# Kernel optimization log

Hardware: AMD Instinct MI355X
Metric: run time of the kernel (lower is better)

Reference implementation:

```python
import jax, jax.numpy as jnp
import numpy as np

NEG_INF_SCALE = -1e9


def multihead(q_in, kv_in, W, b, mask):
    # W: [3, H, d, dh] (q, k, v); b: [3, H, dh]
    q = jnp.einsum('bsd,hdk->bhsk', q_in, W[0]) + b[0][None, :, None, :]
    k = jnp.einsum('bsd,hdk->bhsk', kv_in, W[1]) + b[1][None, :, None, :]
    v = jnp.einsum('bsd,hdk->bhsk', kv_in, W[2]) + b[2][None, :, None, :]
    dh = q.shape[-1]
    scores = jnp.einsum('bhqd,bhkd->bhqk', q, k) / jnp.sqrt(jnp.float32(dh))
    if mask is not None:
        scores = scores + mask * NEG_INF_SCALE  # mask==1 at disallowed positions
    attn = jax.nn.softmax(scores, axis=-1)
    out = jnp.einsum('bhqk,bhkd->bhqd', attn, v)
    B, H, S, DH = out.shape
    # concat of per-head outputs along last axis == transpose + reshape
    return out.transpose(0, 2, 1, 3).reshape(B, S, H * DH)


def setup_inputs() -> dict:
    key = jax.random.key(0)
    ks = jax.random.split(key, 8)
    B, S, D, H, DH, DFF = 8, 1024, 1024, 16, 64, 2048
    sc_in = 1.0 / np.sqrt(D)
    sc_ff = 1.0 / np.sqrt(DFF)
    de_x = jax.random.normal(ks[0], (B, S, D), jnp.float32)
    en_x = jax.random.normal(ks[1], (B, S, D), jnp.float32)
    # causal mask: 1 at masked (future) positions
    mask = jnp.triu(jnp.ones((S, S), jnp.float32), k=1)
    attn1_w = jax.random.normal(ks[2], (3, H, D, DH), jnp.float32) * sc_in
    attn1_b = jnp.zeros((3, H, DH), jnp.float32)
    attn2_w = jax.random.normal(ks[3], (3, H, D, DH), jnp.float32) * sc_in
    attn2_b = jnp.zeros((3, H, DH), jnp.float32)
    ffn_w1 = jax.random.normal(ks[4], (D, DFF), jnp.float32) * sc_in
    ffn_b1 = jnp.zeros((DFF,), jnp.float32)
    ffn_w2 = jax.random.normal(ks[5], (DFF, D), jnp.float32) * sc_ff
    ffn_b2 = jnp.zeros((D,), jnp.float32)
    return {'de_x': de_x, 'en_x': en_x, 'mask': mask,
            'attn1_w': attn1_w, 'attn1_b': attn1_b,
            'attn2_w': attn2_w, 'attn2_b': attn2_b,
            'ffn_w1': ffn_w1, 'ffn_b1': ffn_b1,
            'ffn_w2': ffn_w2, 'ffn_b2': ffn_b2}


def reference(de_x, en_x, mask, attn1_w, attn1_b, attn2_w, attn2_b,
              ffn_w1, ffn_b1, ffn_w2, ffn_b2):
    # block 1: K=V=en_x, Q=de_x, masked (as in source: head(en_x, en_x, de_x, mask))
    h1 = multihead(de_x, en_x, attn1_w, attn1_b, mask)
    # block 2: K=V=en_x, Q=h1, no mask
    h2 = multihead(h1, en_x, attn2_w, attn2_b, None)
    # FCLayer(2048, d): d -> 2048 relu -> d
    y = jax.nn.relu(h2 @ ffn_w1 + ffn_b1) @ ffn_w2 + ffn_b2
    return y
```

## Files before the change

kernel.cpp:

```cpp
#include <hip/hip_runtime.h>

typedef unsigned short u16;
typedef __attribute__((ext_vector_type(8))) __bf16 bf16x8;
typedef __attribute__((ext_vector_type(4))) float f32x4;

__device__ __forceinline__ u16 f2bf(float f) {
    unsigned int u = __builtin_bit_cast(unsigned int, f);
    u = (u + 0x7fffu + ((u >> 16) & 1u)) >> 16;
    return (u16)u;
}

typedef __attribute__((address_space(1))) const void gv_t;
typedef __attribute__((address_space(3))) void lv_t;
__device__ __forceinline__ void gl_lds16(const void* g, void* l) {
    __builtin_amdgcn_global_load_lds((gv_t*)g, (lv_t*)l, 16, 0, 0);
}

__global__ __launch_bounds__(256) void cvt_bf16_k(const float* __restrict__ in,
                                                  u16* __restrict__ out, int n4) {
    int i = blockIdx.x * 256 + threadIdx.x;
    if (i >= n4) return;
    float4 f = ((const float4*)in)[i];
    ushort4 o;
    o.x = f2bf(f.x); o.y = f2bf(f.y); o.z = f2bf(f.z); o.w = f2bf(f.w);
    ((ushort4*)out)[i] = o;
}

__global__ __launch_bounds__(256) void pack_attn_w_k(const float* __restrict__ W,
                                                     u16* __restrict__ out) {
    int idx = blockIdx.x * 256 + threadIdx.x;
    int kk = idx & 63;
    int d  = (idx >> 6) & 1023;
    int h  = (idx >> 16) & 15;
    int p  = idx >> 20;
    out[p * 1048576 + (h * 64 + kk) * 1024 + d] = f2bf(W[idx]);
}

__global__ __launch_bounds__(256) void transpose_bf16_k(const float* __restrict__ in,
                                                        u16* __restrict__ out, int R, int C) {
    int idx = blockIdx.x * 256 + threadIdx.x;
    if (idx >= R * C) return;
    int r = idx / C, c = idx - r * C;
    out[c * R + r] = f2bf(in[idx]);
}

__device__ __forceinline__ void g256_core(const u16* __restrict__ Ab,
                                          const u16* __restrict__ Bb,
                                          int K, u16* __restrict__ As,
                                          u16* __restrict__ Bs,
                                          f32x4 (&acc)[8][4]) {
    const int tid = threadIdx.x, lane = tid & 63, wid = tid >> 6;
    const int wm = wid >> 2, wn = wid & 3;
    const int l15 = lane & 15, l4 = lane >> 4;
    const int gsw = (lane & 7) ^ ((lane >> 3) & 7);
    const int lr = lane >> 3;

    bf16x8 a[4][2], b[2][2];

#define STG(MATb, MATs, buf, half, kt) { \
    _Pragma("unroll") \
    for (int j = 0; j < 2; ++j) { \
        const int r = (half) * 128 + j * 64 + wid * 8; \
        gl_lds16(MATb + (size_t)(r + lr) * K + (kt) * 64 + gsw * 8, \
                 &MATs[(buf) * 16384 + r * 64]); \
    } }
#define LDA(buf, MLO) { \
    _Pragma("unroll") \
    for (int mf = 0; mf < 4; ++mf) \
    _Pragma("unroll") \
    for (int ks = 0; ks < 2; ++ks) \
        a[mf][ks] = *(const bf16x8*)&As[(buf) * 16384 \
            + (wm * 128 + ((MLO) + mf) * 16 + l15) * 64 \
            + (((ks * 4 + l4) ^ (l15 & 7)) * 8)]; \
    }
#define LDB(buf, NLO) { \
    _Pragma("unroll") \
    for (int nf = 0; nf < 2; ++nf) \
    _Pragma("unroll") \
    for (int ks = 0; ks < 2; ++ks) \
        b[nf][ks] = *(const bf16x8*)&Bs[(buf) * 16384 \
            + (wn * 64 + ((NLO) + nf) * 16 + l15) * 64 \
            + (((ks * 4 + l4) ^ (l15 & 7)) * 8)]; \
    }
#define MMA(MLO, NLO) { \
    __builtin_amdgcn_s_setprio(1); \
    _Pragma("unroll") \
    for (int mf = 0; mf < 4; ++mf) \
    _Pragma("unroll") \
    for (int nf = 0; nf < 2; ++nf) \
    _Pragma("unroll") \
    for (int ks = 0; ks < 2; ++ks) \
        acc[(MLO) + mf][(NLO) + nf] = __builtin_amdgcn_mfma_f32_16x16x32_bf16( \
            a[mf][ks], b[nf][ks], acc[(MLO) + mf][(NLO) + nf], 0, 0, 0); \
    __builtin_amdgcn_s_setprio(0); \
    }
#define BARR __builtin_amdgcn_s_barrier()
#define LGKM0 { asm volatile("s_waitcnt lgkmcnt(0)" ::: "memory"); \
                __builtin_amdgcn_sched_barrier(0); }
#define WTV2 asm volatile("s_waitcnt vmcnt(2)" ::: "memory")
#define WTV0 asm volatile("s_waitcnt vmcnt(0)" ::: "memory")

    const int NI = K >> 7;
    STG(Ab, As, 0, 0, 0); STG(Ab, As, 0, 1, 0);
    STG(Bb, Bs, 0, 0, 0); STG(Bb, Bs, 0, 1, 0);
    STG(Ab, As, 1, 0, 1);
    WTV2;
    BARR;

    for (int it = 0; it < NI; ++it) {
        const int t1 = 2 * it + 1, t2 = 2 * it + 2, t3 = 2 * it + 3;
        const bool nl = (it + 1 < NI);
        LDA(0, 0); LDB(0, 0);
        STG(Ab, As, 1, 1, t1);
        BARR; LGKM0; MMA(0, 0); BARR;
        LDB(0, 2);
        STG(Bb, Bs, 1, 0, t1);
        BARR; LGKM0; MMA(0, 2); BARR;
        LDA(0, 4); LDB(0, 0);
        STG(Bb, Bs, 1, 1, t1);
        BARR; LGKM0; MMA(4, 0); BARR;
        LDB(0, 2);
        if (nl) STG(Ab, As, 0, 0, t2);
        BARR; LGKM0; MMA(4, 2);
        if (nl) { WTV2; } else { WTV0; }
        BARR;
        LDA(1, 0); LDB(1, 0);
        if (nl) STG(Ab, As, 0, 1, t2);
        BARR; LGKM0; MMA(0, 0); BARR;
        LDB(1, 2);
        if (nl) STG(Bb, Bs, 0, 0, t2);
        BARR; LGKM0; MMA(0, 2); BARR;
        LDA(1, 4); LDB(1, 0);
        if (nl) STG(Bb, Bs, 0, 1, t2);
        BARR; LGKM0; MMA(4, 0); BARR;
        LDB(1, 2);
        if (nl) STG(Ab, As, 1, 0, t3);
        BARR; LGKM0; MMA(4, 2);
        if (nl) WTV2;
        BARR;
    }
#undef STG
#undef LDA
#undef LDB
#undef MMA
#undef BARR
#undef LGKM0
#undef WTV2
#undef WTV0
}

template <int MODE>
__global__ __launch_bounds__(512, 2) void gemm256_k(const u16* __restrict__ A,
        const u16* __restrict__ Bt, const float* __restrict__ bias,
        u16* __restrict__ Obf, float* __restrict__ Of,
        int M, int N, int K, float scale) {
    __shared__ u16 As[32768];
    __shared__ u16 Bs[32768];
    const int m0 = blockIdx.y * 256, n0 = blockIdx.x * 256;
    f32x4 acc[8][4] = {};
    g256_core(A + (size_t)m0 * K, Bt + (size_t)n0 * K, K, As, Bs, acc);

    const int lane = threadIdx.x & 63, wid = threadIdx.x >> 6;
    const int wm = wid >> 2, wn = wid & 3, l15 = lane & 15, l4 = lane >> 4;
    #pragma unroll
    for (int mf = 0; mf < 8; ++mf)
        #pragma unroll
        for (int nf = 0; nf < 4; ++nf) {
            int col = n0 + wn * 64 + nf * 16 + l15;
            float bv = bias[col];
            int row0 = m0 + wm * 128 + mf * 16 + l4 * 4;
            #pragma unroll
            for (int i = 0; i < 4; ++i) {
                float v = acc[mf][nf][i] + bv;
                if (MODE == 1) v = fmaxf(v, 0.f);
                v *= scale;
                if (MODE == 2) Of[(size_t)(row0 + i) * N + col] = v;
                else           Obf[(size_t)(row0 + i) * N + col] = f2bf(v);
            }
        }
}

__global__ __launch_bounds__(512, 2) void gemm256_proj_k(const u16* __restrict__ Ade,
        const u16* __restrict__ Aen, const u16* __restrict__ W,
        const float* __restrict__ b1, const float* __restrict__ b2,
        u16* __restrict__ Qb, u16* __restrict__ Kb1, u16* __restrict__ Vt1,
        u16* __restrict__ Kb2, u16* __restrict__ Vt2) {
    const int K = 1024;
    __shared__ u16 As[32768];
    __shared__ u16 Bs[32768];
    const int xt = blockIdx.x;
    const int n0 = (xt < 12 ? xt : xt + 4) * 256;
    const int seg = n0 >> 10;
    const int m0 = blockIdx.y * 256;
    const u16* A = (seg == 0) ? Ade : Aen;
    f32x4 acc[8][4] = {};
    g256_core(A + (size_t)m0 * K, W + (size_t)n0 * K, K, As, Bs, acc);

    const int lane = threadIdx.x & 63, wid = threadIdx.x >> 6;
    const int wm = wid >> 2, wn = wid & 3, l15 = lane & 15, l4 = lane >> 4;
    const float* bias = (seg < 3) ? (b1 + seg * 1024) : (b2 + (seg - 3) * 1024);
    const int isV = (seg == 2 || seg == 5);
    u16* Orow = (seg == 0) ? Qb : (seg == 1 ? Kb1 : Kb2);
    u16* Ovt  = (seg == 2) ? Vt1 : Vt2;
    const float scale = (seg == 0) ? 0.125f : 1.0f;

    #pragma unroll
    for (int mf = 0; mf < 8; ++mf)
        #pragma unroll
        for (int nf = 0; nf < 4; ++nf) {
            int colg = n0 + wn * 64 + nf * 16 + l15;
            int col = colg & 1023;
            float bv = bias[col];
            int row0 = m0 + wm * 128 + mf * 16 + l4 * 4;
            if (isV) {
                ushort4 o;
                o.x = f2bf(acc[mf][nf][0] + bv);
                o.y = f2bf(acc[mf][nf][1] + bv);
                o.z = f2bf(acc[mf][nf][2] + bv);
                o.w = f2bf(acc[mf][nf][3] + bv);
                size_t off = ((size_t)((row0 >> 10) * 16 + (col >> 6)) * 64
                              + (col & 63)) * 1024 + (row0 & 1023);
                *(ushort4*)&Ovt[off] = o;
            } else {
                #pragma unroll
                for (int i = 0; i < 4; ++i)
                    Orow[(size_t)(row0 + i) * 1024 + col] =
                        f2bf((acc[mf][nf][i] + bv) * scale);
            }
        }
}

template <int CAUSAL>
__global__ __launch_bounds__(256) void attn_k(const u16* __restrict__ Q,
                                              const u16* __restrict__ Kg_,
                                              const u16* __restrict__ Vt_,
                                              u16* __restrict__ O, int S) {
    const int HD = 1024;
    __shared__ u16 Kl[2][4096];
    __shared__ u16 Vl[2][4096];
    __shared__ u16 Pl[4][16 * 72];
    const int tid = threadIdx.x, lane = tid & 63, w = tid >> 6;
    const int qt = blockIdx.x, h = blockIdx.y, b = blockIdx.z;
    const u16* Qg  = Q   + ((size_t)b * S) * HD + h * 64;
    const u16* Kgp = Kg_ + ((size_t)b * S) * HD + h * 64;
    const u16* Vtp = Vt_ + (size_t)(b * 16 + h) * 64 * 1024;
    const int q0 = qt * 64 + w * 16;
    const int l15 = lane & 15, l4 = lane >> 4;
    const int sr = lane >> 3, sc = lane & 7;

    bf16x8 aq[2];
    #pragma unroll
    for (int kc = 0; kc < 2; ++kc)
        aq[kc] = *(const bf16x8*)&Qg[(size_t)(q0 + l15) * HD + kc * 32 + l4 * 8];

    f32x4 acc_o[4] = {};
    float mrow[4], lrow[4];
    #pragma unroll
    for (int i = 0; i < 4; ++i) { mrow[i] = -3.0e38f; lrow[i] = 0.f; }
    u16* Pw = Pl[w];

    const int nkb = CAUSAL ? (qt + 1) : (S / 64);

    {
        #pragma unroll
        for (int qq = 0; qq < 2; ++qq) {
            int rbase = w * 16 + qq * 8;
            int r = rbase + sr;
            int cs = sc ^ (r & 7);
            gl_lds16(Kgp + (size_t)r * HD + cs * 8, (void*)&Kl[0][rbase * 64]);
            gl_lds16(Vtp + (size_t)r * 1024 + cs * 8, (void*)&Vl[0][rbase * 64]);
        }
    }
    __syncthreads();

    int buf = 0;
    for (int kb = 0; kb < nkb; ++kb) {
        if (kb + 1 < nkb) {
            const int k0n = (kb + 1) * 64;
            #pragma unroll
            for (int qq = 0; qq < 2; ++qq) {
                int rbase = w * 16 + qq * 8;
                int r = rbase + sr;
                int cs = sc ^ (r & 7);
                gl_lds16(Kgp + (size_t)(k0n + r) * HD + cs * 8, (void*)&Kl[buf ^ 1][rbase * 64]);
                gl_lds16(Vtp + (size_t)r * 1024 + k0n + cs * 8, (void*)&Vl[buf ^ 1][rbase * 64]);
            }
        }
        const u16* Kc = Kl[buf];
        const u16* Vc = Vl[buf];

        f32x4 accs[4] = {};
        #pragma unroll
        for (int ct = 0; ct < 4; ++ct) {
            int row = ct * 16 + l15;
            #pragma unroll
            for (int kc = 0; kc < 2; ++kc) {
                int g = kc * 4 + l4;
                bf16x8 bk = *(const bf16x8*)&Kc[row * 64 + (g ^ (row & 7)) * 8];
                accs[ct] = __builtin_amdgcn_mfma_f32_16x16x32_bf16(aq[kc], bk, accs[ct], 0, 0, 0);
            }
        }

        float vals[4][4], tmax[4];
        #pragma unroll
        for (int i = 0; i < 4; ++i) tmax[i] = -3.0e38f;
        if (CAUSAL && kb == qt) {
            #pragma unroll
            for (int ct = 0; ct < 4; ++ct)
                #pragma unroll
                for (int i = 0; i < 4; ++i) {
                    float v = accs[ct][i];
                    int kr = ct * 16 + l15;
                    int qr = w * 16 + l4 * 4 + i;
                    if (kr > qr) v = -1.0e9f;
                    vals[ct][i] = v;
                    tmax[i] = fmaxf(tmax[i], v);
                }
        } else {
            #pragma unroll
            for (int ct = 0; ct < 4; ++ct)
                #pragma unroll
                for (int i = 0; i < 4; ++i) {
                    float v = accs[ct][i];
                    vals[ct][i] = v;
                    tmax[i] = fmaxf(tmax[i], v);
                }
        }
        #pragma unroll
        for (int off = 1; off < 16; off <<= 1)
            #pragma unroll
            for (int i = 0; i < 4; ++i) tmax[i] = fmaxf(tmax[i], __shfl_xor(tmax[i], off));

        float scale[4], rsum[4];
        #pragma unroll
        for (int i = 0; i < 4; ++i) {
            float mn = fmaxf(mrow[i], tmax[i]);
            scale[i] = __expf(mrow[i] - mn);
            mrow[i] = mn;
            rsum[i] = 0.f;
        }
        #pragma unroll
        for (int ct = 0; ct < 4; ++ct)
            #pragma unroll
            for (int i = 0; i < 4; ++i) {
                float p = __expf(vals[ct][i] - mrow[i]);
                vals[ct][i] = p;
                rsum[i] += p;
            }
        #pragma unroll
        for (int off = 1; off < 16; off <<= 1)
            #pragma unroll
            for (int i = 0; i < 4; ++i) rsum[i] += __shfl_xor(rsum[i], off);
        #pragma unroll
        for (int i = 0; i < 4; ++i) lrow[i] = lrow[i] * scale[i] + rsum[i];
        #pragma unroll
        for (int dt = 0; dt < 4; ++dt)
            #pragma unroll
            for (int i = 0; i < 4; ++i) acc_o[dt][i] *= scale[i];

        #pragma unroll
        for (int ct = 0; ct < 4; ++ct)
            #pragma unroll
            for (int i = 0; i < 4; ++i)
                Pw[(l4 * 4 + i) * 72 + ct * 16 + l15] = f2bf(vals[ct][i]);

        #pragma unroll
        for (int kc2 = 0; kc2 < 2; ++kc2) {
            bf16x8 pa = *(const bf16x8*)&Pw[l15 * 72 + kc2 * 32 + l4 * 8];
            #pragma unroll
            for (int dt = 0; dt < 4; ++dt) {
                int row = dt * 16 + l15;
                int g = kc2 * 4 + l4;
                bf16x8 bv = *(const bf16x8*)&Vc[row * 64 + (g ^ (row & 7)) * 8];
                acc_o[dt] = __builtin_amdgcn_mfma_f32_16x16x32_bf16(pa, bv, acc_o[dt], 0, 0, 0);
            }
        }
        __syncthreads();
        buf ^= 1;
    }

    #pragma unroll
    for (int dt = 0; dt < 4; ++dt)
        #pragma unroll
        for (int i = 0; i < 4; ++i) {
            float o = acc_o[dt][i] / lrow[i];
            O[(size_t)(b * S + q0 + l4 * 4 + i) * HD + h * 64 + dt * 16 + l15] = f2bf(o);
        }
}

extern "C" void kernel_launch(void* const* d_in, const int* in_sizes, int n_in,
                              void* d_out, int out_size, void* d_ws, size_t ws_size,
                              hipStream_t stream) {
    const float* de_x = (const float*)d_in[0];
    const float* en_x = (const float*)d_in[1];
    const float* a1w  = (const float*)d_in[3];
    const float* a1b  = (const float*)d_in[4];
    const float* a2w  = (const float*)d_in[5];
    const float* a2b  = (const float*)d_in[6];
    const float* fw1  = (const float*)d_in[7];
    const float* fb1  = (const float*)d_in[8];
    const float* fw2  = (const float*)d_in[9];
    const float* fb2  = (const float*)d_in[10];
    float* out = (float*)d_out;
    u16* ws = (u16*)d_ws;

    u16* bf_de = ws + 0;
    u16* bf_en = ws + 8388608;
    u16* wproj = ws + 16777216;
    u16* wf1t  = ws + 23068672;
    u16* wf2t  = ws + 25165824;
    u16* Qb    = ws + 27262976;
    u16* Kb1   = ws + 35651584;
    u16* Vt1   = ws + 44040192;
    u16* Kb2   = ws + 52428800;
    u16* Vt2   = ws + 60817408;
    u16* h1  = bf_en;
    u16* h2  = bf_de;
    u16* mid = Kb1;
    if (ws_size < (size_t)69206016 * 2) return;

    dim3 blk(256);

    cvt_bf16_k<<<8192, blk, 0, stream>>>(de_x, bf_de, 2097152);
    cvt_bf16_k<<<8192, blk, 0, stream>>>(en_x, bf_en, 2097152);
    pack_attn_w_k<<<12288, blk, 0, stream>>>(a1w, wproj);
    pack_attn_w_k<<<12288, blk, 0, stream>>>(a2w, wproj + 3145728);
    transpose_bf16_k<<<8192, blk, 0, stream>>>(fw1, wf1t, 1024, 2048);
    transpose_bf16_k<<<8192, blk, 0, stream>>>(fw2, wf2t, 2048, 1024);

    gemm256_proj_k<<<dim3(20, 32), 512, 0, stream>>>(bf_de, bf_en, wproj, a1b, a2b,
                                                     Qb, Kb1, Vt1, Kb2, Vt2);
    attn_k<1><<<dim3(16, 16, 8), blk, 0, stream>>>(Qb, Kb1, Vt1, h1, 1024);

    gemm256_k<0><<<dim3(4, 32), 512, 0, stream>>>(h1, wproj + 3145728, a2b,
                                                  Qb, nullptr, 8192, 1024, 1024, 0.125f);
    attn_k<0><<<dim3(16, 16, 8), blk, 0, stream>>>(Qb, Kb2, Vt2, h2, 1024);

    gemm256_k<1><<<dim3(8, 32), 512, 0, stream>>>(h2, wf1t, fb1, mid, nullptr,
                                                  8192, 2048, 1024, 1.0f);
    gemm256_k<2><<<dim3(4, 32), 512, 0, stream>>>(mid, wf2t, fb2, nullptr, out,
                                                  8192, 1024, 2048, 1.0f);
}
```

Before: 700.3 us.

## Retile attention to 128 queries, rework GEMM staging, tiled weight transposes

```diff
diff --git a/kernel.cpp b/kernel.cpp
--- a/kernel.cpp
+++ b/kernel.cpp
@@ -26,22 +26,22 @@
     ((ushort4*)out)[i] = o;
 }
 
-__global__ __launch_bounds__(256) void pack_attn_w_k(const float* __restrict__ W,
-                                                     u16* __restrict__ out) {
-    int idx = blockIdx.x * 256 + threadIdx.x;
-    int kk = idx & 63;
-    int d  = (idx >> 6) & 1023;
-    int h  = (idx >> 16) & 15;
-    int p  = idx >> 20;
-    out[p * 1048576 + (h * 64 + kk) * 1024 + d] = f2bf(W[idx]);
-}
-
-__global__ __launch_bounds__(256) void transpose_bf16_k(const float* __restrict__ in,
-                                                        u16* __restrict__ out, int R, int C) {
-    int idx = blockIdx.x * 256 + threadIdx.x;
-    if (idx >= R * C) return;
-    int r = idx / C, c = idx - r * C;
-    out[c * R + r] = f2bf(in[idx]);
+__global__ __launch_bounds__(256) void transpose_pack_k(const float* __restrict__ in,
+                                                        u16* __restrict__ out,
+                                                        int R, int C) {
+    __shared__ float t[32][33];
+    const size_t slab = (size_t)blockIdx.z * R * C;
+    in  += slab;
+    out += slab;
+    const int c0 = blockIdx.x * 32, r0 = blockIdx.y * 32;
+    const int tx = threadIdx.x & 31, ty = threadIdx.x >> 5;
+    #pragma unroll
+    for (int j = 0; j < 32; j += 8)
+        t[ty + j][tx] = in[(size_t)(r0 + ty + j) * C + c0 + tx];
+    __syncthreads();
+    #pragma unroll
+    for (int j = 0; j < 32; j += 8)
+        out[(size_t)(c0 + ty + j) * R + r0 + tx] = f2bf(t[tx][ty + j]);
 }
 
 __device__ __forceinline__ void g256_core(const u16* __restrict__ Ab,
@@ -55,7 +55,7 @@
     const int gsw = (lane & 7) ^ ((lane >> 3) & 7);
     const int lr = lane >> 3;
 
-    bf16x8 a[4][2], b[2][2];
+    bf16x8 a[4][2], b[4][2];
 
 #define STG(MATb, MATs, buf, half, kt) { \
     _Pragma("unroll") \
@@ -78,7 +78,7 @@
     for (int nf = 0; nf < 2; ++nf) \
     _Pragma("unroll") \
     for (int ks = 0; ks < 2; ++ks) \
-        b[nf][ks] = *(const bf16x8*)&Bs[(buf) * 16384 \
+        b[(NLO) + nf][ks] = *(const bf16x8*)&Bs[(buf) * 16384 \
             + (wn * 64 + ((NLO) + nf) * 16 + l15) * 64 \
             + (((ks * 4 + l4) ^ (l15 & 7)) * 8)]; \
     }
@@ -91,52 +91,49 @@
     _Pragma("unroll") \
     for (int ks = 0; ks < 2; ++ks) \
         acc[(MLO) + mf][(NLO) + nf] = __builtin_amdgcn_mfma_f32_16x16x32_bf16( \
-            a[mf][ks], b[nf][ks], acc[(MLO) + mf][(NLO) + nf], 0, 0, 0); \
+            a[mf][ks], b[(NLO) + nf][ks], acc[(MLO) + mf][(NLO) + nf], 0, 0, 0); \
     __builtin_amdgcn_s_setprio(0); \
     }
 #define BARR __builtin_amdgcn_s_barrier()
 #define LGKM0 { asm volatile("s_waitcnt lgkmcnt(0)" ::: "memory"); \
                 __builtin_amdgcn_sched_barrier(0); }
-#define WTV2 asm volatile("s_waitcnt vmcnt(2)" ::: "memory")
+#define WTV6 asm volatile("s_waitcnt vmcnt(6)" ::: "memory")
+#define WTV8 asm volatile("s_waitcnt vmcnt(8)" ::: "memory")
 #define WTV0 asm volatile("s_waitcnt vmcnt(0)" ::: "memory")
 
     const int NI = K >> 7;
     STG(Ab, As, 0, 0, 0); STG(Ab, As, 0, 1, 0);
     STG(Bb, Bs, 0, 0, 0); STG(Bb, Bs, 0, 1, 0);
-    STG(Ab, As, 1, 0, 1);
-    WTV2;
+    STG(Ab, As, 1, 0, 1); STG(Ab, As, 1, 1, 1);
+    STG(Bb, Bs, 1, 0, 1); STG(Bb, Bs, 1, 1, 1);
+    WTV8;
     BARR;
 
     for (int it = 0; it < NI; ++it) {
-        const int t1 = 2 * it + 1, t2 = 2 * it + 2, t3 = 2 * it + 3;
+        const int t2 = 2 * it + 2, t3 = 2 * it + 3;
         const bool nl = (it + 1 < NI);
         LDA(0, 0); LDB(0, 0);
-        STG(Ab, As, 1, 1, t1);
         BARR; LGKM0; MMA(0, 0); BARR;
         LDB(0, 2);
-        STG(Bb, Bs, 1, 0, t1);
         BARR; LGKM0; MMA(0, 2); BARR;
-        LDA(0, 4); LDB(0, 0);
-        STG(Bb, Bs, 1, 1, t1);
-        BARR; LGKM0; MMA(4, 0); BARR;
-        LDB(0, 2);
-        if (nl) STG(Ab, As, 0, 0, t2);
-        BARR; LGKM0; MMA(4, 2);
-        if (nl) { WTV2; } else { WTV0; }
+        LDA(0, 4);
+        if (nl) STG(Bb, Bs, 0, 0, t2);
+        BARR; LGKM0; MMA(4, 2); BARR;
+        if (nl) { STG(Ab, As, 0, 0, t2); STG(Bb, Bs, 0, 1, t2); }
+        BARR; MMA(4, 0);
+        if (nl) { WTV6; } else { WTV0; }
         BARR;
         LDA(1, 0); LDB(1, 0);
         if (nl) STG(Ab, As, 0, 1, t2);
         BARR; LGKM0; MMA(0, 0); BARR;
         LDB(1, 2);
-        if (nl) STG(Bb, Bs, 0, 0, t2);
         BARR; LGKM0; MMA(0, 2); BARR;
-        LDA(1, 4); LDB(1, 0);
-        if (nl) STG(Bb, Bs, 0, 1, t2);
-        BARR; LGKM0; MMA(4, 0); BARR;
-        LDB(1, 2);
-        if (nl) STG(Ab, As, 1, 0, t3);
-        BARR; LGKM0; MMA(4, 2);
-        if (nl) WTV2;
+        LDA(1, 4);
+        if (nl) STG(Bb, Bs, 1, 0, t3);
+        BARR; LGKM0; MMA(4, 2); BARR;
+        if (nl) { STG(Ab, As, 1, 0, t3); STG(Ab, As, 1, 1, t3); STG(Bb, Bs, 1, 1, t3); }
+        BARR; MMA(4, 0);
+        if (nl) WTV8;
         BARR;
     }
 #undef STG
@@ -145,7 +142,8 @@
 #undef MMA
 #undef BARR
 #undef LGKM0
-#undef WTV2
+#undef WTV6
+#undef WTV8
 #undef WTV0
 }
 
@@ -231,22 +229,25 @@
 }
 
 template <int CAUSAL>
-__global__ __launch_bounds__(256) void attn_k(const u16* __restrict__ Q,
+__global__ __launch_bounds__(512) void attn_k(const u16* __restrict__ Q,
                                               const u16* __restrict__ Kg_,
                                               const u16* __restrict__ Vt_,
                                               u16* __restrict__ O, int S) {
     const int HD = 1024;
     __shared__ u16 Kl[2][4096];
     __shared__ u16 Vl[2][4096];
-    __shared__ u16 Pl[4][16 * 72];
+    __shared__ u16 Pl[8][16 * 72];
     const int tid = threadIdx.x, lane = tid & 63, w = tid >> 6;
     const int qt = blockIdx.x, h = blockIdx.y, b = blockIdx.z;
     const u16* Qg  = Q   + ((size_t)b * S) * HD + h * 64;
     const u16* Kgp = Kg_ + ((size_t)b * S) * HD + h * 64;
     const u16* Vtp = Vt_ + (size_t)(b * 16 + h) * 64 * 1024;
-    const int q0 = qt * 64 + w * 16;
+    const int q0 = qt * 128 + w * 16;
     const int l15 = lane & 15, l4 = lane >> 4;
     const int sr = lane >> 3, sc = lane & 7;
+    const int rbase = w * 8;
+    const int r = rbase + sr;
+    const int cs = sc ^ (r & 7);
 
     bf16x8 aq[2];
     #pragma unroll
@@ -259,32 +260,18 @@
     for (int i = 0; i < 4; ++i) { mrow[i] = -3.0e38f; lrow[i] = 0.f; }
     u16* Pw = Pl[w];
 
-    const int nkb = CAUSAL ? (qt + 1) : (S / 64);
-
-    {
-        #pragma unroll
-        for (int qq = 0; qq < 2; ++qq) {
-            int rbase = w * 16 + qq * 8;
-            int r = rbase + sr;
-            int cs = sc ^ (r & 7);
-            gl_lds16(Kgp + (size_t)r * HD + cs * 8, (void*)&Kl[0][rbase * 64]);
-            gl_lds16(Vtp + (size_t)r * 1024 + cs * 8, (void*)&Vl[0][rbase * 64]);
-        }
-    }
+    const int nkb = CAUSAL ? (2 * qt + 2) : (S / 64);
+
+    gl_lds16(Kgp + (size_t)r * HD + cs * 8, (void*)&Kl[0][rbase * 64]);
+    gl_lds16(Vtp + (size_t)r * 1024 + cs * 8, (void*)&Vl[0][rbase * 64]);
     __syncthreads();
 
     int buf = 0;
     for (int kb = 0; kb < nkb; ++kb) {
         if (kb + 1 < nkb) {
             const int k0n = (kb + 1) * 64;
-            #pragma unroll
-            for (int qq = 0; qq < 2; ++qq) {
-                int rbase = w * 16 + qq * 8;
-                int r = rbase + sr;
-                int cs = sc ^ (r & 7);
-                gl_lds16(Kgp + (size_t)(k0n + r) * HD + cs * 8, (void*)&Kl[buf ^ 1][rbase * 64]);
-                gl_lds16(Vtp + (size_t)r * 1024 + k0n + cs * 8, (void*)&Vl[buf ^ 1][rbase * 64]);
-            }
+            gl_lds16(Kgp + (size_t)(k0n + r) * HD + cs * 8, (void*)&Kl[buf ^ 1][rbase * 64]);
+            gl_lds16(Vtp + (size_t)r * 1024 + k0n + cs * 8, (void*)&Vl[buf ^ 1][rbase * 64]);
         }
         const u16* Kc = Kl[buf];
         const u16* Vc = Vl[buf];
@@ -304,15 +291,15 @@
         float vals[4][4], tmax[4];
         #pragma unroll
         for (int i = 0; i < 4; ++i) tmax[i] = -3.0e38f;
-        if (CAUSAL && kb == qt) {
+        if (CAUSAL && kb >= 2 * qt) {
             #pragma unroll
             for (int ct = 0; ct < 4; ++ct)
                 #pragma unroll
                 for (int i = 0; i < 4; ++i) {
                     float v = accs[ct][i];
-                    int kr = ct * 16 + l15;
-                    int qr = w * 16 + l4 * 4 + i;
-                    if (kr > qr) v = -1.0e9f;
+                    int kg = kb * 64 + ct * 16 + l15;
+                    int qg = q0 + l4 * 4 + i;
+                    if (kg > qg) v = -1.0e9f;
                     vals[ct][i] = v;
                     tmax[i] = fmaxf(tmax[i], v);
                 }
@@ -423,18 +410,18 @@
 
     cvt_bf16_k<<<8192, blk, 0, stream>>>(de_x, bf_de, 2097152);
     cvt_bf16_k<<<8192, blk, 0, stream>>>(en_x, bf_en, 2097152);
-    pack_attn_w_k<<<12288, blk, 0, stream>>>(a1w, wproj);
-    pack_attn_w_k<<<12288, blk, 0, stream>>>(a2w, wproj + 3145728);
-    transpose_bf16_k<<<8192, blk, 0, stream>>>(fw1, wf1t, 1024, 2048);
-    transpose_bf16_k<<<8192, blk, 0, stream>>>(fw2, wf2t, 2048, 1024);
+    transpose_pack_k<<<dim3(2, 32, 48), blk, 0, stream>>>(a1w, wproj, 1024, 64);
+    transpose_pack_k<<<dim3(2, 32, 48), blk, 0, stream>>>(a2w, wproj + 3145728, 1024, 64);
+    transpose_pack_k<<<dim3(64, 32, 1), blk, 0, stream>>>(fw1, wf1t, 1024, 2048);
+    transpose_pack_k<<<dim3(32, 64, 1), blk, 0, stream>>>(fw2, wf2t, 2048, 1024);
 
     gemm256_proj_k<<<dim3(20, 32), 512, 0, stream>>>(bf_de, bf_en, wproj, a1b, a2b,
                                                      Qb, Kb1, Vt1, Kb2, Vt2);
-    attn_k<1><<<dim3(16, 16, 8), blk, 0, stream>>>(Qb, Kb1, Vt1, h1, 1024);
+    attn_k<1><<<dim3(8, 16, 8), 512, 0, stream>>>(Qb, Kb1, Vt1, h1, 1024);
 
     gemm256_k<0><<<dim3(4, 32), 512, 0, stream>>>(h1, wproj + 3145728, a2b,
                                                   Qb, nullptr, 8192, 1024, 1024, 0.125f);
-    attn_k<0><<<dim3(16, 16, 8), blk, 0, stream>>>(Qb, Kb2, Vt2, h2, 1024);
+    attn_k<0><<<dim3(8, 16, 8), 512, 0, stream>>>(Qb, Kb2, Vt2, h2, 1024);
 
     gemm256_k<1><<<dim3(8, 32), 512, 0, stream>>>(h2, wf1t, fb1, mid, nullptr,
                                                   8192, 2048, 1024, 1.0f);
```

Result: faster. 608.6 us (-13.1%).
